# Performance work log

Hardware: AMD Instinct MI355X
Metric: run time of the kernel (lower is better)

Reference implementation:

```python
import jax, jax.numpy as jnp
import numpy as np

B, S, E = 2, 2048, 4096
H, KV, D = 32, 8, 128  # heads, kv heads, head_dim
ROPE_BASE = 500000.0


def setup_inputs() -> dict:
    key = jax.random.key(0)
    ks = jax.random.split(key, 5)
    scale = 0.02
    return {
        "x": jax.random.normal(ks[0], (B, S, E), dtype=jnp.float32),
        "wq": jax.random.normal(ks[1], (E, E), dtype=jnp.float32) * scale,
        "wk": jax.random.normal(ks[2], (KV * D, E), dtype=jnp.float32) * scale,
        "wv": jax.random.normal(ks[3], (KV * D, E), dtype=jnp.float32) * scale,
        "wo": jax.random.normal(ks[4], (E, E), dtype=jnp.float32) * scale,
        "input_pos": jnp.arange(S, dtype=jnp.int64 if jax.config.jax_enable_x64 else jnp.int32),
    }


def _rope(xh, input_pos):
    # xh: [B, H, S, D]; standard llama rotate-half RoPE
    half = D // 2
    inv_freq = 1.0 / (ROPE_BASE ** (jnp.arange(0, half, dtype=jnp.float32) / half))
    ang = input_pos.astype(jnp.float32)[:, None] * inv_freq[None, :]  # [S, half]
    cos, sin = jnp.cos(ang), jnp.sin(ang)
    x1, x2 = xh[..., :half], xh[..., half:]
    return jnp.concatenate([x1 * cos - x2 * sin, x2 * cos + x1 * sin], axis=-1)


def reference(x, wq, wk, wv, wo, input_pos):
    bsz, seq_len, _ = x.shape
    q = (x @ wq.T).reshape(bsz, seq_len, H, D).transpose(0, 2, 1, 3)    # [B,H,S,D]
    k = (x @ wk.T).reshape(bsz, seq_len, KV, D).transpose(0, 2, 1, 3)   # [B,KV,S,D]
    v = (x @ wv.T).reshape(bsz, seq_len, KV, D).transpose(0, 2, 1, 3)
    # repeat_kv: B (H R) S D with R = H // KV
    rep = H // KV
    k = jnp.repeat(k, rep, axis=1)
    v = jnp.repeat(v, rep, axis=1)
    q = _rope(q, input_pos)
    k = _rope(k, input_pos)
    # causal SDPA
    scores = jnp.einsum("bhqd,bhkd->bhqk", q, k) / jnp.sqrt(jnp.float32(D))
    causal = jnp.tril(jnp.ones((seq_len, seq_len), dtype=bool))
    scores = jnp.where(causal, scores, jnp.finfo(scores.dtype).min)
    probs = jax.nn.softmax(scores, axis=-1)
    out = jnp.einsum("bhqk,bhkd->bhqd", probs, v)                       # [B,H,S,D]
    out = out.transpose(0, 2, 1, 3).reshape(bsz, seq_len, E)
    return out @ wo.T
```

## Files before the change

kernel.cpp:

```cpp
#include <hip/hip_runtime.h>

#define B_ 2
#define S_ 2048
#define E_ 4096
#define H_ 32
#define KV_ 8
#define D_ 128

typedef __bf16 v8bf __attribute__((ext_vector_type(8)));
typedef __bf16 v4bf __attribute__((ext_vector_type(4)));
typedef float  v4f  __attribute__((ext_vector_type(4)));

static __device__ __forceinline__ v4f mfma16(v8bf a, v8bf b, v4f c) {
    return __builtin_amdgcn_mfma_f32_16x16x32_bf16(a, b, c, 0, 0, 0);
}

static __device__ __forceinline__ void load_lds16(const void* g, void* l) {
    __builtin_amdgcn_global_load_lds(
        (const __attribute__((address_space(1))) void*)g,
        (__attribute__((address_space(3))) void*)l, 16, 0, 0);
}

__global__ __launch_bounds__(256) void cast_f32_to_bf16(
        const float4* __restrict__ in, v4bf* __restrict__ out, int n4) {
    int i = blockIdx.x * blockDim.x + threadIdx.x;
    if (i >= n4) return;
    float4 v = in[i];
    v4bf o;
    o[0] = (__bf16)v.x; o[1] = (__bf16)v.y; o[2] = (__bf16)v.z; o[3] = (__bf16)v.w;
    out[i] = o;
}

__global__ __launch_bounds__(256) void rope_inplace(
        __bf16* __restrict__ qk, const int* __restrict__ pos, int nh,
        int rowstride, float outscale) {
    int idx = blockIdx.x * blockDim.x + threadIdx.x;
    int d = idx & 63;
    int t = idx >> 6;
    int h = t % nh;
    int bs = t / nh;
    if (bs >= B_ * S_) return;
    int s = bs & (S_ - 1);
    float p = (float)pos[s];
    float inv = expf(-(float)d * (1.0f / 64.0f) * 13.122363377404329f);
    float ang = p * inv;
    float c = cosf(ang), sn = sinf(ang);
    size_t off = (size_t)bs * rowstride + (size_t)h * D_;
    float x1 = (float)qk[off + d];
    float x2 = (float)qk[off + d + 64];
    qk[off + d]      = (__bf16)((x1 * c - x2 * sn) * outscale);
    qk[off + d + 64] = (__bf16)((x2 * c + x1 * sn) * outscale);
}

template <int EPI>
__global__ __launch_bounds__(512, 2) void gemm_bt(
        const __bf16* __restrict__ A, const __bf16* __restrict__ Bm,
        void* __restrict__ Cv, void* __restrict__ Cv2, int M, int N, int K) {
    __shared__ __bf16 As[2][256 * 64];
    __shared__ __bf16 Bs[2][256 * 64];
    const int tid  = threadIdx.x;
    const int wave = tid >> 6;
    const int lane = tid & 63;
    const int l15  = lane & 15;
    const int quad = lane >> 4;

    const int nbx = N >> 8;
    const int nwg = (int)gridDim.x;
    const int swz = ((int)blockIdx.x & 7) * (nwg >> 3) + ((int)blockIdx.x >> 3);
    const int bm  = (swz / nbx) * 256;
    const int bn  = (swz % nbx) * 256;

    const int wr = wave >> 2;
    const int wc = wave & 3;

    v4f acc[8][4] = {};

    const int srow = wave * 8 + (lane >> 3);
    const int scc  = (lane & 7) ^ ((lane >> 3) & 7);

    auto stage = [&](int t, int buf) {
        const size_t k0 = (size_t)t * 64;
#pragma unroll
        for (int g = 0; g < 4; ++g) {
            load_lds16(A + (size_t)(bm + g * 64 + srow) * K + k0 + scc * 8,
                       (char*)&As[buf][0] + (size_t)g * 8192 + (size_t)wave * 1024);
            load_lds16(Bm + (size_t)(bn + g * 64 + srow) * K + k0 + scc * 8,
                       (char*)&Bs[buf][0] + (size_t)g * 8192 + (size_t)wave * 1024);
        }
    };

    stage(0, 0);

    const int nt = K >> 6;
    for (int t = 0; t < nt; ++t) {
        const int cur = t & 1;
        if (t + 1 < nt) {
            stage(t + 1, cur ^ 1);
            asm volatile("s_waitcnt vmcnt(8)" ::: "memory");
        } else {
            asm volatile("s_waitcnt vmcnt(0)" ::: "memory");
        }
        __builtin_amdgcn_s_barrier();
        __builtin_amdgcn_sched_barrier(0);

        const __bf16* Asc = &As[cur][0];
        const __bf16* Bsc = &Bs[cur][0];
        v8bf a[4][2], b0[2][2], b1[2][2];

#pragma unroll
        for (int i = 0; i < 4; ++i)
#pragma unroll
            for (int kk = 0; kk < 2; ++kk)
                a[i][kk] = *(const v8bf*)&Asc[
                    (wr * 128 + i * 16 + l15) * 64 +
                    (((kk * 4 + quad) ^ (l15 & 7)) * 8)];
#pragma unroll
        for (int j = 0; j < 2; ++j)
#pragma unroll
            for (int kk = 0; kk < 2; ++kk) {
                b0[j][kk] = *(const v8bf*)&Bsc[
                    (wc * 64 + j * 16 + l15) * 64 +
                    (((kk * 4 + quad) ^ (l15 & 7)) * 8)];
                b1[j][kk] = *(const v8bf*)&Bsc[
                    (wc * 64 + 32 + j * 16 + l15) * 64 +
                    (((kk * 4 + quad) ^ (l15 & 7)) * 8)];
            }

        __builtin_amdgcn_s_setprio(1);
#pragma unroll
        for (int kk = 0; kk < 2; ++kk)
#pragma unroll
            for (int i = 0; i < 4; ++i)
#pragma unroll
                for (int j = 0; j < 2; ++j)
                    acc[i][j] = mfma16(a[i][kk], b0[j][kk], acc[i][j]);
#pragma unroll
        for (int kk = 0; kk < 2; ++kk)
#pragma unroll
            for (int i = 0; i < 4; ++i)
#pragma unroll
                for (int j = 0; j < 2; ++j)
                    acc[i][2 + j] = mfma16(a[i][kk], b1[j][kk], acc[i][2 + j]);
        __builtin_amdgcn_s_setprio(0);

#pragma unroll
        for (int i = 0; i < 4; ++i)
#pragma unroll
            for (int kk = 0; kk < 2; ++kk)
                a[i][kk] = *(const v8bf*)&Asc[
                    (wr * 128 + 64 + i * 16 + l15) * 64 +
                    (((kk * 4 + quad) ^ (l15 & 7)) * 8)];

        __builtin_amdgcn_s_setprio(1);
#pragma unroll
        for (int kk = 0; kk < 2; ++kk)
#pragma unroll
            for (int i = 0; i < 4; ++i)
#pragma unroll
                for (int j = 0; j < 2; ++j)
                    acc[4 + i][2 + j] = mfma16(a[i][kk], b1[j][kk], acc[4 + i][2 + j]);
#pragma unroll
        for (int kk = 0; kk < 2; ++kk)
#pragma unroll
            for (int i = 0; i < 4; ++i)
#pragma unroll
                for (int j = 0; j < 2; ++j)
                    acc[4 + i][j] = mfma16(a[i][kk], b0[j][kk], acc[4 + i][j]);
        __builtin_amdgcn_s_setprio(0);

        __builtin_amdgcn_sched_barrier(0);
        asm volatile("s_waitcnt lgkmcnt(0)" ::: "memory");
        __builtin_amdgcn_s_barrier();
        __builtin_amdgcn_sched_barrier(0);
    }

#pragma unroll
    for (int mi = 0; mi < 8; ++mi) {
#pragma unroll
        for (int nj = 0; nj < 4; ++nj) {
#pragma unroll
            for (int r = 0; r < 4; ++r) {
                int row = bm + wr * 128 + mi * 16 + quad * 4 + r;
                int col = bn + wc * 64 + nj * 16 + l15;
                float val = acc[mi][nj][r];
                if (EPI == 0) {
                    ((float*)Cv)[(size_t)row * N + col] = val;
                } else if (EPI == 1) {
                    ((__bf16*)Cv)[(size_t)row * N + col] = (__bf16)val;
                } else {
                    if (col < 1024) {
                        ((__bf16*)Cv)[(size_t)row * 1024 + col] = (__bf16)val;
                    } else {
                        int cc = col - 1024;
                        int b  = row >> 11, s = row & (S_ - 1);
                        int kv = cc >> 7,  d = cc & (D_ - 1);
                        ((__bf16*)Cv2)[((size_t)((b * KV_ + kv) * D_ + d)) * S_ + s] = (__bf16)val;
                    }
                }
            }
        }
    }
}

__global__ __launch_bounds__(256, 2) void attn_fused(
        const __bf16* __restrict__ q, const __bf16* __restrict__ k,
        const __bf16* __restrict__ vt, __bf16* __restrict__ attn) {
    __shared__ __bf16 Ks[2][64 * 128];
    __shared__ __bf16 Vs[2][128 * 64];
    __shared__ __bf16 P[4][16 * 64];
    const int wave = threadIdx.x >> 6;
    const int lane = threadIdx.x & 63;

    const int wgid = blockIdx.x;
    const int xcd  = wgid & 7;
    const int slot = wgid >> 3;
    const int bh   = xcd * 8 + (slot >> 5);
    const int qblk = 31 - (slot & 31);
    const int b = bh >> 5;
    const int h = bh & 31;
    const int kvh = h >> 2;
    const int q0 = qblk * 64 + wave * 16;
    const int l15  = lane & 15;
    const int quad = lane >> 4;

    const __bf16* qbase = q  + (size_t)(b * S_) * E_ + (size_t)h * D_;
    const __bf16* kbase = k  + (size_t)(b * S_) * (KV_ * D_) + (size_t)kvh * D_;
    const __bf16* vbase = vt + (size_t)((b * KV_ + kvh) * D_) * S_;
    __bf16* Pw = &P[wave][0];

    const int krow_l = lane >> 4;
    const int kcc    = lane & 15;
    const int vrow_l = lane >> 3;
    const int vcc    = lane & 7;

    auto stageK = [&](int t, int buf) {
#pragma unroll
        for (int i = 0; i < 4; ++i) {
            int g = wave * 4 + i;
            int row = g * 4 + krow_l;
            int scc = kcc ^ (row & 15);
            load_lds16(kbase + (size_t)(t * 64 + row) * (KV_ * D_) + scc * 8,
                       (char*)&Ks[buf][0] + (size_t)g * 1024);
        }
    };
    auto stageV = [&](int t, int buf) {
#pragma unroll
        for (int i = 0; i < 4; ++i) {
            int g = wave * 4 + i;
            int row = g * 8 + vrow_l;
            int scc = vcc ^ (row & 7);
            load_lds16(vbase + (size_t)row * S_ + t * 64 + scc * 8,
                       (char*)&Vs[buf][0] + (size_t)g * 1024);
        }
    };

    stageK(0, 0);
    stageV(0, 0);

    v8bf aq[4];
#pragma unroll
    for (int kc = 0; kc < 4; ++kc)
        aq[kc] = *(const v8bf*)(qbase + (size_t)(q0 + l15) * E_ + kc * 32 + quad * 8);

    v4f o[8] = {};
    float m_i = -INFINITY, l_i = 0.f;

    const int ntiles = qblk + 1;

    for (int t = 0; t < ntiles; ++t) {
        const int cur = t & 1;
        if (t + 1 < ntiles) {
            stageK(t + 1, cur ^ 1);
            stageV(t + 1, cur ^ 1);
            asm volatile("s_waitcnt vmcnt(8)" ::: "memory");
        } else {
            asm volatile("s_waitcnt vmcnt(0)" ::: "memory");
        }
        __builtin_amdgcn_s_barrier();
        __builtin_amdgcn_sched_barrier(0);

        const int n0 = t * 64;
        const __bf16* Ksc = &Ks[cur][0];
        const __bf16* Vsc = &Vs[cur][0];

        v4f s[4] = {};
        __builtin_amdgcn_s_setprio(1);
#pragma unroll
        for (int kc = 0; kc < 4; ++kc) {
            v8bf kf[4];
#pragma unroll
            for (int j = 0; j < 4; ++j)
                kf[j] = *(const v8bf*)&Ksc[(j * 16 + l15) * 128 +
                                           (((kc * 4 + quad) ^ l15) * 8)];
#pragma unroll
            for (int j = 0; j < 4; ++j)
                s[j] = mfma16(kf[j], aq[kc], s[j]);
        }
        __builtin_amdgcn_s_setprio(0);

        float e[4][4];
        if (n0 + 63 > q0) {
#pragma unroll
            for (int j = 0; j < 4; ++j)
#pragma unroll
                for (int r = 0; r < 4; ++r) {
                    float v = s[j][r];
                    if (n0 + j * 16 + quad * 4 + r > q0 + l15) v = -INFINITY;
                    e[j][r] = v;
                }
        } else {
#pragma unroll
            for (int j = 0; j < 4; ++j)
#pragma unroll
                for (int r = 0; r < 4; ++r)
                    e[j][r] = s[j][r];
        }

        float mloc = e[0][0];
#pragma unroll
        for (int j = 0; j < 4; ++j)
#pragma unroll
            for (int r = 0; r < 4; ++r)
                mloc = fmaxf(mloc, e[j][r]);
        mloc = fmaxf(mloc, __shfl_xor(mloc, 16, 64));
        mloc = fmaxf(mloc, __shfl_xor(mloc, 32, 64));

        if (!__all(mloc - m_i <= 8.0f)) {
            float mnew = fmaxf(m_i, mloc);
            float alpha = __expf(m_i - mnew);
            m_i = mnew;
            l_i *= alpha;
            float af[4];
#pragma unroll
            for (int r = 0; r < 4; ++r)
                af[r] = __shfl(alpha, quad * 4 + r, 16);
#pragma unroll
            for (int c = 0; c < 8; ++c)
#pragma unroll
                for (int r = 0; r < 4; ++r)
                    o[c][r] *= af[r];
        }

        float psum = 0.f;
#pragma unroll
        for (int j = 0; j < 4; ++j)
#pragma unroll
            for (int r = 0; r < 4; ++r) {
                e[j][r] = __expf(e[j][r] - m_i);
                psum += e[j][r];
            }
        psum += __shfl_xor(psum, 16, 64);
        psum += __shfl_xor(psum, 32, 64);
        l_i += psum;

#pragma unroll
        for (int j = 0; j < 4; ++j) {
            v4bf pk;
#pragma unroll
            for (int r = 0; r < 4; ++r) pk[r] = (__bf16)e[j][r];
            int cl = j * 2 + (quad >> 1);
            *(v4bf*)&Pw[l15 * 64 + ((cl ^ (l15 & 7)) << 3) + ((quad & 1) << 2)] = pk;
        }

        v8bf ap0 = *(const v8bf*)&Pw[l15 * 64 + ((quad ^ (l15 & 7)) << 3)];
        v8bf ap1 = *(const v8bf*)&Pw[l15 * 64 + (((4 + quad) ^ (l15 & 7)) << 3)];

        __builtin_amdgcn_s_setprio(1);
#pragma unroll
        for (int c = 0; c < 8; ++c) {
            v8bf v0 = *(const v8bf*)&Vsc[(c * 16 + l15) * 64 +
                                         ((quad ^ (l15 & 7)) * 8)];
            v8bf v1 = *(const v8bf*)&Vsc[(c * 16 + l15) * 64 +
                                         (((4 + quad) ^ (l15 & 7)) * 8)];
            o[c] = mfma16(ap0, v0, o[c]);
            o[c] = mfma16(ap1, v1, o[c]);
        }
        __builtin_amdgcn_s_setprio(0);

        __builtin_amdgcn_sched_barrier(0);
        asm volatile("s_waitcnt lgkmcnt(0)" ::: "memory");
        __builtin_amdgcn_s_barrier();
        __builtin_amdgcn_sched_barrier(0);
    }

    float linv = 1.0f / l_i;
    float lr[4];
#pragma unroll
    for (int r = 0; r < 4; ++r)
        lr[r] = __shfl(linv, quad * 4 + r, 16);
    __bf16* obase = attn + (size_t)(b * S_) * E_ + (size_t)h * D_;
#pragma unroll
    for (int c = 0; c < 8; ++c)
#pragma unroll
        for (int r = 0; r < 4; ++r)
            obase[(size_t)(q0 + quad * 4 + r) * E_ + c * 16 + l15] =
                (__bf16)(o[c][r] * lr[r]);
}

extern "C" void kernel_launch(void* const* d_in, const int* in_sizes, int n_in,
                              void* d_out, int out_size, void* d_ws, size_t ws_size,
                              hipStream_t stream) {
    (void)in_sizes; (void)n_in; (void)out_size; (void)ws_size;
    const float* x  = (const float*)d_in[0];
    const float* wq = (const float*)d_in[1];
    const float* wk = (const float*)d_in[2];
    const float* wv = (const float*)d_in[3];
    const float* wo = (const float*)d_in[4];
    const int*   pos = (const int*)d_in[5];
    float* out = (float*)d_out;

    char* ws = (char*)d_ws;
    size_t off = 0;
    auto alloc = [&](size_t bytes) {
        char* p = ws + off;
        off += (bytes + 255) & ~(size_t)255;
        return p;
    };
    __bf16* xb   = (__bf16*)alloc((size_t)B_ * S_ * E_ * 2);
    __bf16* wqb  = (__bf16*)alloc((size_t)E_ * E_ * 2);
    __bf16* wkvb = (__bf16*)alloc((size_t)2 * KV_ * D_ * E_ * 2);
    __bf16* wob  = (__bf16*)alloc((size_t)E_ * E_ * 2);
    __bf16* qb   = (__bf16*)alloc((size_t)B_ * S_ * E_ * 2);
    __bf16* kb   = (__bf16*)alloc((size_t)B_ * S_ * KV_ * D_ * 2);
    __bf16* vt   = (__bf16*)alloc((size_t)B_ * KV_ * D_ * S_ * 2);
    __bf16* at   = (__bf16*)alloc((size_t)B_ * S_ * E_ * 2);

    auto cast = [&](const float* in, __bf16* ob, size_t n) {
        int n4 = (int)(n / 4);
        cast_f32_to_bf16<<<(n4 + 255) / 256, 256, 0, stream>>>(
            (const float4*)in, (v4bf*)ob, n4);
    };
    cast(x,  xb,  (size_t)B_ * S_ * E_);
    cast(wq, wqb, (size_t)E_ * E_);
    cast(wk, wkvb, (size_t)KV_ * D_ * E_);
    cast(wv, wkvb + (size_t)KV_ * D_ * E_, (size_t)KV_ * D_ * E_);
    cast(wo, wob, (size_t)E_ * E_);

    const int M = B_ * S_;
    const int nwg_e = (E_ / 256) * (M / 256);
    const int nwg_kv = (2 * KV_ * D_ / 256) * (M / 256);
    gemm_bt<1><<<dim3(nwg_e), 512, 0, stream>>>(
        xb, wqb, qb, nullptr, M, E_, E_);
    gemm_bt<2><<<dim3(nwg_kv), 512, 0, stream>>>(
        xb, wkvb, kb, vt, M, 2 * KV_ * D_, E_);

    rope_inplace<<<(B_ * S_ * H_ * 64 + 255) / 256, 256, 0, stream>>>(
        qb, pos, H_, E_, 0.08838834764831845f);
    rope_inplace<<<(B_ * S_ * KV_ * 64 + 255) / 256, 256, 0, stream>>>(
        kb, pos, KV_, KV_ * D_, 1.0f);

    attn_fused<<<dim3(B_ * H_ * (S_ / 64)), 256, 0, stream>>>(qb, kb, vt, at);

    gemm_bt<0><<<dim3(nwg_e), 512, 0, stream>>>(
        at, wob, out, nullptr, M, E_, E_);
}
```

Before: 816.1 us.

## Split GEMM LDS tiles into quarter tiles with staggered per-quarter prefetch

Reorganizes the GEMM shared-memory staging into four half-tiles (A top, B left, B right, A bottom) per buffer. Each one is prefetched for the next k-step right after its current data has been read into registers, with finer-grained vmcnt waits and barriers between MFMA phases. This interleaves global-to-LDS loads with MFMA work more evenly than the previous whole-tile double buffer. In exchange it adds several more barriers per iteration, and the hand-tuned vmcnt counts are fragile to get right.

```diff
diff --git a/kernel.cpp b/kernel.cpp
--- a/kernel.cpp
+++ b/kernel.cpp
@@ -56,8 +56,7 @@
 __global__ __launch_bounds__(512, 2) void gemm_bt(
         const __bf16* __restrict__ A, const __bf16* __restrict__ Bm,
         void* __restrict__ Cv, void* __restrict__ Cv2, int M, int N, int K) {
-    __shared__ __bf16 As[2][256 * 64];
-    __shared__ __bf16 Bs[2][256 * 64];
+    __shared__ __bf16 H[2][4][128 * 64];
     const int tid  = threadIdx.x;
     const int wave = tid >> 6;
     const int lane = tid & 63;
@@ -75,57 +74,59 @@
 
     v4f acc[8][4] = {};
 
-    const int srow = wave * 8 + (lane >> 3);
-    const int scc  = (lane & 7) ^ ((lane >> 3) & 7);
-
-    auto stage = [&](int t, int buf) {
-        const size_t k0 = (size_t)t * 64;
-#pragma unroll
-        for (int g = 0; g < 4; ++g) {
-            load_lds16(A + (size_t)(bm + g * 64 + srow) * K + k0 + scc * 8,
-                       (char*)&As[buf][0] + (size_t)g * 8192 + (size_t)wave * 1024);
-            load_lds16(Bm + (size_t)(bn + g * 64 + srow) * K + k0 + scc * 8,
-                       (char*)&Bs[buf][0] + (size_t)g * 8192 + (size_t)wave * 1024);
+    const int srow8 = tid >> 3;
+    const int scc   = (tid & 7) ^ (srow8 & 7);
+
+    auto stageHT = [&](int t, int h) {
+        char* dbase = (char*)&H[t & 1][h][0] + (size_t)wave * 1024;
+        const size_t kof = (size_t)t * 64 + scc * 8;
+        if (h == 0 || h == 3) {
+            const int mh = (h == 3);
+#pragma unroll
+            for (int g = 0; g < 2; ++g) {
+                int row = bm + g * 128 + mh * 64 + srow8;
+                load_lds16(A + (size_t)row * K + kof, dbase + g * 8192);
+            }
+        } else {
+            const int nh = (h == 2);
+#pragma unroll
+            for (int g = 0; g < 2; ++g) {
+                int sc  = g * 64 + srow8;
+                int col = bn + (sc >> 5) * 64 + nh * 32 + (sc & 31);
+                load_lds16(Bm + (size_t)col * K + kof, dbase + g * 8192);
+            }
         }
     };
 
-    stage(0, 0);
+    stageHT(0, 0); stageHT(0, 1); stageHT(0, 2); stageHT(0, 3);
+    asm volatile("s_waitcnt vmcnt(4)" ::: "memory");
+    __builtin_amdgcn_s_barrier();
 
     const int nt = K >> 6;
     for (int t = 0; t < nt; ++t) {
         const int cur = t & 1;
-        if (t + 1 < nt) {
-            stage(t + 1, cur ^ 1);
-            asm volatile("s_waitcnt vmcnt(8)" ::: "memory");
-        } else {
-            asm volatile("s_waitcnt vmcnt(0)" ::: "memory");
-        }
-        __builtin_amdgcn_s_barrier();
-        __builtin_amdgcn_sched_barrier(0);
-
-        const __bf16* Asc = &As[cur][0];
-        const __bf16* Bsc = &Bs[cur][0];
+        const bool more = (t + 1 < nt);
+        const __bf16* A0p = &H[cur][0][0];
+        const __bf16* B0p = &H[cur][1][0];
+        const __bf16* B1p = &H[cur][2][0];
+        const __bf16* A1p = &H[cur][3][0];
         v8bf a[4][2], b0[2][2], b1[2][2];
 
 #pragma unroll
         for (int i = 0; i < 4; ++i)
 #pragma unroll
             for (int kk = 0; kk < 2; ++kk)
-                a[i][kk] = *(const v8bf*)&Asc[
-                    (wr * 128 + i * 16 + l15) * 64 +
-                    (((kk * 4 + quad) ^ (l15 & 7)) * 8)];
+                a[i][kk] = *(const v8bf*)&A0p[(wr * 64 + i * 16 + l15) * 64 +
+                                              (((kk * 4 + quad) ^ (l15 & 7)) * 8)];
 #pragma unroll
         for (int j = 0; j < 2; ++j)
 #pragma unroll
-            for (int kk = 0; kk < 2; ++kk) {
-                b0[j][kk] = *(const v8bf*)&Bsc[
-                    (wc * 64 + j * 16 + l15) * 64 +
-                    (((kk * 4 + quad) ^ (l15 & 7)) * 8)];
-                b1[j][kk] = *(const v8bf*)&Bsc[
-                    (wc * 64 + 32 + j * 16 + l15) * 64 +
-                    (((kk * 4 + quad) ^ (l15 & 7)) * 8)];
-            }
-
+            for (int kk = 0; kk < 2; ++kk)
+                b0[j][kk] = *(const v8bf*)&B0p[(wc * 32 + j * 16 + l15) * 64 +
+                                               (((kk * 4 + quad) ^ (l15 & 7)) * 8)];
+        if (more) stageHT(t + 1, 0);
+        __builtin_amdgcn_s_barrier();
+        asm volatile("s_waitcnt lgkmcnt(0)" ::: "memory");
         __builtin_amdgcn_s_setprio(1);
 #pragma unroll
         for (int kk = 0; kk < 2; ++kk)
@@ -134,6 +135,21 @@
 #pragma unroll
                 for (int j = 0; j < 2; ++j)
                     acc[i][j] = mfma16(a[i][kk], b0[j][kk], acc[i][j]);
+        __builtin_amdgcn_s_setprio(0);
+        if (more) asm volatile("s_waitcnt vmcnt(4)" ::: "memory");
+        else      asm volatile("s_waitcnt vmcnt(2)" ::: "memory");
+        __builtin_amdgcn_s_barrier();
+
+#pragma unroll
+        for (int j = 0; j < 2; ++j)
+#pragma unroll
+            for (int kk = 0; kk < 2; ++kk)
+                b1[j][kk] = *(const v8bf*)&B1p[(wc * 32 + j * 16 + l15) * 64 +
+                                               (((kk * 4 + quad) ^ (l15 & 7)) * 8)];
+        if (more) stageHT(t + 1, 1);
+        __builtin_amdgcn_s_barrier();
+        asm volatile("s_waitcnt lgkmcnt(0)" ::: "memory");
+        __builtin_amdgcn_s_setprio(1);
 #pragma unroll
         for (int kk = 0; kk < 2; ++kk)
 #pragma unroll
@@ -142,15 +158,19 @@
                 for (int j = 0; j < 2; ++j)
                     acc[i][2 + j] = mfma16(a[i][kk], b1[j][kk], acc[i][2 + j]);
         __builtin_amdgcn_s_setprio(0);
+        if (more) asm volatile("s_waitcnt vmcnt(4)" ::: "memory");
+        else      asm volatile("s_waitcnt vmcnt(0)" ::: "memory");
+        __builtin_amdgcn_s_barrier();
 
 #pragma unroll
         for (int i = 0; i < 4; ++i)
 #pragma unroll
             for (int kk = 0; kk < 2; ++kk)
-                a[i][kk] = *(const v8bf*)&Asc[
-                    (wr * 128 + 64 + i * 16 + l15) * 64 +
-                    (((kk * 4 + quad) ^ (l15 & 7)) * 8)];
-
+                a[i][kk] = *(const v8bf*)&A1p[(wr * 64 + i * 16 + l15) * 64 +
+                                              (((kk * 4 + quad) ^ (l15 & 7)) * 8)];
+        if (more) stageHT(t + 1, 2);
+        __builtin_amdgcn_s_barrier();
+        asm volatile("s_waitcnt lgkmcnt(0)" ::: "memory");
         __builtin_amdgcn_s_setprio(1);
 #pragma unroll
         for (int kk = 0; kk < 2; ++kk)
@@ -159,6 +179,12 @@
 #pragma unroll
                 for (int j = 0; j < 2; ++j)
                     acc[4 + i][2 + j] = mfma16(a[i][kk], b1[j][kk], acc[4 + i][2 + j]);
+        __builtin_amdgcn_s_setprio(0);
+        __builtin_amdgcn_s_barrier();
+
+        if (more) stageHT(t + 1, 3);
+        __builtin_amdgcn_s_barrier();
+        __builtin_amdgcn_s_setprio(1);
 #pragma unroll
         for (int kk = 0; kk < 2; ++kk)
 #pragma unroll
@@ -167,11 +193,8 @@
                 for (int j = 0; j < 2; ++j)
                     acc[4 + i][j] = mfma16(a[i][kk], b0[j][kk], acc[4 + i][j]);
         __builtin_amdgcn_s_setprio(0);
-
-        __builtin_amdgcn_sched_barrier(0);
-        asm volatile("s_waitcnt lgkmcnt(0)" ::: "memory");
-        __builtin_amdgcn_s_barrier();
-        __builtin_amdgcn_sched_barrier(0);
+        if (more) asm volatile("s_waitcnt vmcnt(4)" ::: "memory");
+        __builtin_amdgcn_s_barrier();
     }
 
 #pragma unroll
```

New measurement: 764.4 us. 6.3% less time.
